# Performance work log

Hardware: AMD Instinct MI355X
Metric: run time of the kernel (lower is better)

Reference implementation:

```python
import jax, jax.numpy as jnp
import numpy as np

B, S, D = 2, 2048, 512
H = 8
G = 4
LAMBDA_INIT = 0.2  # 0.8 - 0.6*exp(-0.3*(layer_idx-1)) with layer_idx=1
EPS = 1e-5


def setup_inputs() -> dict:
    key = jax.random.key(0)
    ks = jax.random.split(key, 16)
    n = jax.random.normal
    return {
        "x": n(ks[0], (B, S, D), jnp.float32),
        "K1_w": n(ks[1], (D, D), jnp.float32) * 0.02,
        "K1_b": n(ks[2], (D,), jnp.float32) * 0.02,
        "Q1_w": n(ks[3], (D, D), jnp.float32) * 0.02,
        "K2_w": n(ks[4], (D, D), jnp.float32) * 0.02,
        "K2_b": n(ks[5], (D,), jnp.float32) * 0.02,
        "Q2_w": n(ks[6], (D, D), jnp.float32) * 0.02,
        "V_w": n(ks[7], (D, D), jnp.float32) * 0.02,
        "lambda_q1": n(ks[8], (H, 1), jnp.float32),
        "lambda_k1": n(ks[9], (H, 1), jnp.float32),
        "lambda_q2": n(ks[10], (H, 1), jnp.float32),
        "lambda_k2": n(ks[11], (H, 1), jnp.float32),
        "gn_w": jnp.ones((D,), jnp.float32),
        "gn_b": jnp.zeros((D,), jnp.float32),
        "out_w": n(ks[12], (D, D), jnp.float32) * 0.02,
        "out_b": n(ks[13], (D,), jnp.float32) * 0.02,
    }


def reference(x, K1_w, K1_b, Q1_w, K2_w, K2_b, Q2_w, V_w,
              lambda_q1, lambda_k1, lambda_q2, lambda_k2,
              gn_w, gn_b, out_w, out_b):
    b, s, d = x.shape
    hd = d // H

    def heads(t):  # (b,s,d) -> (b,H,s,hd)
        return t.reshape(b, s, H, hd).transpose(0, 2, 1, 3)

    q1 = heads(x @ Q1_w.T)
    k1 = heads(x @ K1_w.T + K1_b)
    q2 = heads(x @ Q2_w.T)
    k2 = heads(x @ K2_w.T + K2_b)
    v = heads(x @ V_w.T)

    scale = hd ** 0.5
    a1 = jax.nn.softmax(jnp.einsum('bhqd,bhkd->bhqk', q1, k1) / scale, axis=-1)
    a2 = jax.nn.softmax(jnp.einsum('bhqd,bhkd->bhqk', q2, k2) / scale, axis=-1)

    lam = (jnp.exp(lambda_q1 * lambda_k1)
           - jnp.exp(lambda_q2 * lambda_k2) + LAMBDA_INIT)  # (H,1)
    attn = a1 - lam.reshape(1, H, 1, 1) * a2

    o = jnp.einsum('bhqk,bhkd->bhqd', attn, v)
    o = o.transpose(0, 2, 1, 3).reshape(b, s, d)

    # GroupNorm over channels: input (b, d, s), groups G normalize over (d/G, s)
    xc = o.transpose(0, 2, 1).reshape(b, G, d // G, s)
    mu = xc.mean(axis=(2, 3), keepdims=True)
    var = xc.var(axis=(2, 3), keepdims=True)
    xn = ((xc - mu) * jax.lax.rsqrt(var + EPS)).reshape(b, d, s)
    xn = xn * gn_w[None, :, None] + gn_b[None, :, None]

    y = xn.transpose(0, 2, 1) @ out_w.T + out_b
    return y
```

## Files before the change

kernel.cpp:

```cpp
#include <hip/hip_runtime.h>
#include <hip/hip_bf16.h>

typedef __bf16 bf16;
typedef __attribute__((ext_vector_type(4))) __bf16 bf16x4;
typedef __attribute__((ext_vector_type(8))) __bf16 bf16x8;
typedef __attribute__((ext_vector_type(4))) float f32x4;

#define MFMA16(a, b, c) __builtin_amdgcn_mfma_f32_16x16x32_bf16((a), (b), (c), 0, 0, 0)

static constexpr float EPS = 1e-5f;
static constexpr float LAMBDA_INIT = 0.2f;
static constexpr float LOG2E = 1.44269504088896340736f;

__device__ __forceinline__ bf16x8 cvt8(const float* p) {
    const f32x4 a = *(const f32x4*)p;
    const f32x4 b = *(const f32x4*)(p + 4);
    bf16x8 r;
    r[0] = (bf16)a[0]; r[1] = (bf16)a[1]; r[2] = (bf16)a[2]; r[3] = (bf16)a[3];
    r[4] = (bf16)b[0]; r[5] = (bf16)b[1]; r[6] = (bf16)b[2]; r[7] = (bf16)b[3];
    return r;
}

__device__ __forceinline__ void gload_lds16(const void* g, void* l) {
    __builtin_amdgcn_global_load_lds(
        (const __attribute__((address_space(1))) unsigned int*)g,
        (__attribute__((address_space(3))) unsigned int*)l,
        16, 0, 0);
}

__global__ __launch_bounds__(256) void prep_kernel(
    const float* __restrict__ x,
    const float* __restrict__ q1w, const float* __restrict__ k1w,
    const float* __restrict__ q2w, const float* __restrict__ k2w,
    const float* __restrict__ vw,
    const float* __restrict__ ow, const float* __restrict__ gnw,
    const float* __restrict__ gnb,
    bf16* __restrict__ xb, bf16* __restrict__ wb,
    bf16* __restrict__ owg, float* __restrict__ S0, float* __restrict__ stats)
{
    const int tid = threadIdx.x;
    if (blockIdx.x < 1664) {
        const size_t base = ((size_t)blockIdx.x * 256 + tid) * 8;
        if (base < 2097152) {
            *(bf16x8*)(xb + base) = cvt8(x + base);
        } else {
            const size_t wbase = base - 2097152;
            const int wsel = (int)(wbase >> 18);
            const size_t off = wbase & 262143;
            const float* W = (wsel == 0) ? q1w : (wsel == 1) ? k1w :
                             (wsel == 2) ? q2w : (wsel == 3) ? k2w : vw;
            *(bf16x8*)(wb + wbase) = cvt8(W + off);
        }
        return;
    }

    __shared__ float red[4];
    const int pb = blockIdx.x - 1664;
    if (pb == 0 && tid < 16) stats[tid] = 0.f;

    const int n0 = pb * 16;
    const int c0 = tid, c1 = tid + 256;
    const float gw0 = gnw[c0], gw1 = gnw[c1];
    const float gb0 = gnb[c0], gb1 = gnb[c1];

    for (int n = 0; n < 16; ++n) {
        const size_t rowb = (size_t)(n0 + n) * 512;
        const float w0 = ow[rowb + c0];
        const float w1 = ow[rowb + c1];
        owg[rowb + c0] = (bf16)(w0 * gw0);
        owg[rowb + c1] = (bf16)(w1 * gw1);
        float s = gb0 * w0 + gb1 * w1;
#pragma unroll
        for (int off = 1; off < 64; off <<= 1) s += __shfl_xor(s, off, 64);
        if ((tid & 63) == 0) red[tid >> 6] = s;
        __syncthreads();
        if (tid == 0) S0[n0 + n] = red[0] + red[1] + red[2] + red[3];
        __syncthreads();
    }
}

__global__ __launch_bounds__(256) void proj_kernel(
    const bf16* __restrict__ xb, const bf16* __restrict__ wb,
    const float* __restrict__ k1b, const float* __restrict__ k2b,
    bf16* __restrict__ q1o, bf16* __restrict__ k1o,
    bf16* __restrict__ q2o, bf16* __restrict__ k2o,
    bf16* __restrict__ vto)
{
    __shared__ __align__(16) bf16 sh[32768];
    bf16* const As0 = sh;
    bf16* const As1 = sh + 8192;
    bf16* const Bs0 = sh + 16384;
    bf16* const Bs1 = sh + 24576;

    const int tid = threadIdx.x;
    const int wave = tid >> 6, lane = tid & 63;
    const int l15 = lane & 15, quad = lane >> 4;
    const int wm = wave >> 1, wn = wave & 1;

    const int mb = blockIdx.x / 20;
    const int nb = blockIdx.x % 20;
    const int wsel = nb >> 2;
    const int nrow0 = (nb & 3) * 128;

    const int srow = lane >> 3;
    const int scol = 8 * ((lane & 7) ^ srow);
    const bf16* ag = xb + (size_t)(mb * 128 + srow) * 512 + scol;
    const bf16* bg = wb + (size_t)(wsel * 512 + nrow0 + srow) * 512 + scol;

    f32x4 acc[4][4];
#pragma unroll
    for (int i = 0; i < 4; ++i)
#pragma unroll
        for (int j = 0; j < 4; ++j)
            acc[i][j] = (f32x4){0.f, 0.f, 0.f, 0.f};

#define STAGE_PROJ(abuf, bbuf, s) do {                                         \
    const int k0_ = (s) * 64;                                                  \
    _Pragma("unroll")                                                          \
    for (int c_ = 0; c_ < 4; ++c_) {                                           \
        const int chunk_ = wave * 4 + c_;                                      \
        gload_lds16(ag + (size_t)(chunk_ * 8) * 512 + k0_, (abuf) + chunk_ * 512); \
        gload_lds16(bg + (size_t)(chunk_ * 8) * 512 + k0_, (bbuf) + chunk_ * 512); \
    }                                                                          \
} while (0)

    STAGE_PROJ(As0, Bs0, 0);
    __syncthreads();

    const int ka = 8 * (quad ^ (l15 & 7));

    for (int s = 0; s < 8; ++s) {
        const bf16* Ac = (s & 1) ? As1 : As0;
        const bf16* Bc = (s & 1) ? Bs1 : Bs0;
        if (s < 7) {
            if (s & 1) STAGE_PROJ(As0, Bs0, s + 1);
            else       STAGE_PROJ(As1, Bs1, s + 1);
        }

        bf16x8 al[4], ah[4], bl[4], bh_[4];
#pragma unroll
        for (int i = 0; i < 4; ++i) {
            const bf16* p = Ac + (wm * 64 + i * 16 + l15) * 64;
            al[i] = *(const bf16x8*)(p + ka);
            ah[i] = *(const bf16x8*)(p + (ka ^ 32));
        }
#pragma unroll
        for (int j = 0; j < 4; ++j) {
            const bf16* p = Bc + (wn * 64 + j * 16 + l15) * 64;
            bl[j]  = *(const bf16x8*)(p + ka);
            bh_[j] = *(const bf16x8*)(p + (ka ^ 32));
        }

#pragma unroll
        for (int i = 0; i < 4; ++i)
#pragma unroll
            for (int j = 0; j < 4; ++j) {
                acc[i][j] = MFMA16(al[i], bl[j], acc[i][j]);
                acc[i][j] = MFMA16(ah[i], bh_[j], acc[i][j]);
            }

        __syncthreads();
    }

    const int bidx = mb >> 4;
    const int sbase = (mb & 15) * 128;
    const float scale = (wsel == 0 || wsel == 2) ? 0.125f * LOG2E : 1.0f;

    if (wsel != 4) {
        bf16* const T = sh;
        const int swzq = quad << 4;
#pragma unroll
        for (int j = 0; j < 4; ++j) {
            const int nl = wn * 64 + j * 16 + l15;
            const int ncol = nrow0 + nl;
            float bias = 0.f;
            if (wsel == 1) bias = k1b[ncol];
            if (wsel == 3) bias = k2b[ncol];
            const int nswz = nl ^ swzq;
#pragma unroll
            for (int i = 0; i < 4; ++i) {
                const int mbase = wm * 64 + i * 16 + quad * 4;
#pragma unroll
                for (int r = 0; r < 4; ++r)
                    T[(mbase + r) * 128 + nswz] = (bf16)(acc[i][j][r] * scale + bias);
            }
        }
        __syncthreads();

        bf16* const dst = (wsel == 0) ? q1o : (wsel == 1) ? k1o :
                          (wsel == 2) ? q2o : k2o;
#pragma unroll
        for (int hsel = 0; hsel < 2; ++hsel) {
            const int h = (nrow0 >> 6) + hsel;
            bf16* db = dst + ((size_t)(bidx * 8 + h) * 2048 + sbase) * 64;
#pragma unroll
            for (int ps = 0; ps < 4; ++ps) {
                const int idx = (ps * 256 + tid) * 8;
                const int m = idx >> 6, hd = idx & 63;
                const bf16x8 v = *(const bf16x8*)(
                    T + m * 128 + ((hsel * 64 + hd) ^ (((m >> 2) & 3) << 4)));
                *(bf16x8*)(db + idx) = v;
            }
        }
    } else {
        bf16* const Tt = sh;
#pragma unroll
        for (int j = 0; j < 4; ++j) {
            const int nl = wn * 64 + j * 16 + l15;
            const int hd = (nrow0 + nl) & 63;
            const int xh = (hd >> 1) & 3;
            const int swz = (nl & 7) << 2;
#pragma unroll
            for (int i = 0; i < 4; ++i) {
                const int colb = (wm * 64 + (i >> 1) * 32 + ((quad ^ xh) << 3)
                                  + ((i & 1) << 2)) ^ swz;
                bf16x4 pk;
#pragma unroll
                for (int r = 0; r < 4; ++r) pk[r] = (bf16)acc[i][j][r];
                *(bf16x4*)(Tt + nl * 132 + colb) = pk;
            }
        }
        __syncthreads();

#pragma unroll
        for (int ps = 0; ps < 8; ++ps) {
            const int rown = ps * 16 + (tid >> 4);
            const int seg = tid & 15;
            const int swz = (rown & 7) << 2;
            const bf16x4 lo = *(const bf16x4*)(Tt + rown * 132 + ((seg * 8) ^ swz));
            const bf16x4 hi = *(const bf16x4*)(Tt + rown * 132 + ((seg * 8 + 4) ^ swz));
            const int ncol = nrow0 + rown;
            const int h = ncol >> 6, hd = ncol & 63;
            bf16x8 v;
            v[0] = lo[0]; v[1] = lo[1]; v[2] = lo[2]; v[3] = lo[3];
            v[4] = hi[0]; v[5] = hi[1]; v[6] = hi[2]; v[7] = hi[3];
            *(bf16x8*)(vto + ((size_t)(bidx * 8 + h) * 64 + hd) * 2048
                       + sbase + seg * 8) = v;
        }
    }
#undef STAGE_PROJ
}

__global__ __launch_bounds__(512, 4) void attn_kernel(
    const bf16* __restrict__ q1, const bf16* __restrict__ k1,
    const bf16* __restrict__ q2, const bf16* __restrict__ k2,
    const bf16* __restrict__ vt,
    const float* __restrict__ lq1, const float* __restrict__ lk1,
    const float* __restrict__ lq2, const float* __restrict__ lk2,
    bf16* __restrict__ o, float* __restrict__ stats)
{
    __shared__ __align__(16) bf16 smem[3][12288];
    __shared__ float lbuf[8][2][16];
    __shared__ float sred[8][2];

    const int tid = threadIdx.x;
    const int wave = tid >> 6;
    const int lane = tid & 63;
    const int l15 = lane & 15, quad = lane >> 4;
    const int qtile = wave & 3;
    const int kg = wave >> 2;

    const int rid = (blockIdx.x & 7) * 64 + (blockIdx.x >> 3);
    const int bh = rid >> 5;
    const int qt = rid & 31;
    const int b = bh >> 3, h = bh & 7;

    const bf16* k1t = k1 + (size_t)bh * 2048 * 64;
    const bf16* k2t = k2 + (size_t)bh * 2048 * 64;
    const bf16* vtt = vt + (size_t)bh * 64 * 2048;

    const int qrow = qt * 64 + qtile * 16 + l15;
    const bf16* q1p = q1 + ((size_t)bh * 2048 + qrow) * 64 + quad * 8;
    const bf16* q2p = q2 + ((size_t)bh * 2048 + qrow) * 64 + quad * 8;
    const bf16x8 q1f0 = *(const bf16x8*)(q1p);
    const bf16x8 q1f1 = *(const bf16x8*)(q1p + 32);
    const bf16x8 q2f0 = *(const bf16x8*)(q2p);
    const bf16x8 q2f1 = *(const bf16x8*)(q2p + 32);

    const int sw = wave & 3;
    const int skey0 = (wave < 4) ? 0 : 1024;
    const size_t ksrc0 = (size_t)(skey0 + sw * 8 + (lane >> 3)) * 64
                       + 8 * ((lane & 7) ^ (lane >> 3));
    const size_t vsrc0 = (size_t)(sw * 16 + (lane >> 2)) * 2048 + skey0 + (lane & 3) * 8;

#define STAGE_ATTN(buf, itv) do {                                   \
    const size_t koff_ = ksrc0 + (size_t)(itv) * 32 * 64;           \
    gload_lds16(k1t + koff_, (buf) + wave * 512);                   \
    gload_lds16(k2t + koff_, (buf) + 4096 + wave * 512);            \
    gload_lds16(vtt + vsrc0 + (itv) * 32, (buf) + 8192 + wave * 512); \
} while (0)

    const int koffa = 8 * (quad ^ (l15 & 7));
    const int koffb = 8 * ((quad + 4) ^ (l15 & 7));
    const int vsw = 8 * (quad ^ ((l15 >> 1) & 3));

    f32x4 O1[4], O2[4];
    float l1 = 0.f, l2 = 0.f;
#pragma unroll
    for (int t = 0; t < 4; ++t) {
        O1[t] = (f32x4){0.f, 0.f, 0.f, 0.f};
        O2[t] = (f32x4){0.f, 0.f, 0.f, 0.f};
    }

    STAGE_ATTN(smem[0], 0);
    STAGE_ATTN(smem[1], 1);

    int cur = 0;
    for (int it = 0; it < 32; ++it) {
        if (it < 31) {
            asm volatile("s_waitcnt vmcnt(3)\ns_barrier" ::: "memory");
        } else {
            asm volatile("s_waitcnt vmcnt(0)\ns_barrier" ::: "memory");
        }
        __builtin_amdgcn_sched_barrier(0);

        const bf16* sb = smem[cur];
        const int n2 = (cur == 0) ? 2 : cur - 1;
        if (it < 30) STAGE_ATTN(smem[n2], it + 2);

        const bf16* k1r = sb + kg * 2048;
        const bf16* k2r = sb + 4096 + kg * 2048;
        const bf16* vr  = sb + 8192 + kg * 2048;

        const bf16x8 k1t0a = *(const bf16x8*)(k1r + l15 * 64 + koffa);
        const bf16x8 k1t0b = *(const bf16x8*)(k1r + l15 * 64 + koffb);
        const bf16x8 k1t1a = *(const bf16x8*)(k1r + (16 + l15) * 64 + koffa);
        const bf16x8 k1t1b = *(const bf16x8*)(k1r + (16 + l15) * 64 + koffb);
        const bf16x8 k2t0a = *(const bf16x8*)(k2r + l15 * 64 + koffa);
        const bf16x8 k2t0b = *(const bf16x8*)(k2r + l15 * 64 + koffb);
        const bf16x8 k2t1a = *(const bf16x8*)(k2r + (16 + l15) * 64 + koffa);
        const bf16x8 k2t1b = *(const bf16x8*)(k2r + (16 + l15) * 64 + koffb);
        const bf16x8 v0 = *(const bf16x8*)(vr + l15 * 32 + vsw);
        const bf16x8 v1 = *(const bf16x8*)(vr + (16 + l15) * 32 + vsw);
        const bf16x8 v2 = *(const bf16x8*)(vr + (32 + l15) * 32 + vsw);
        const bf16x8 v3 = *(const bf16x8*)(vr + (48 + l15) * 32 + vsw);

        const f32x4 z = (f32x4){0.f, 0.f, 0.f, 0.f};
        __builtin_amdgcn_s_setprio(1);
        f32x4 s1t0 = MFMA16(k1t0a, q1f0, z);  s1t0 = MFMA16(k1t0b, q1f1, s1t0);
        f32x4 s1t1 = MFMA16(k1t1a, q1f0, z);  s1t1 = MFMA16(k1t1b, q1f1, s1t1);
        f32x4 s2t0 = MFMA16(k2t0a, q2f0, z);  s2t0 = MFMA16(k2t0b, q2f1, s2t0);
        f32x4 s2t1 = MFMA16(k2t1a, q2f0, z);  s2t1 = MFMA16(k2t1b, q2f1, s2t1);
        __builtin_amdgcn_s_setprio(0);

        bf16x8 b1, b2;
#pragma unroll
        for (int r = 0; r < 4; ++r) {
            float e;
            e = __builtin_amdgcn_exp2f(s1t0[r]); l1 += e; b1[r]     = (bf16)e;
            e = __builtin_amdgcn_exp2f(s1t1[r]); l1 += e; b1[4 + r] = (bf16)e;
            e = __builtin_amdgcn_exp2f(s2t0[r]); l2 += e; b2[r]     = (bf16)e;
            e = __builtin_amdgcn_exp2f(s2t1[r]); l2 += e; b2[4 + r] = (bf16)e;
        }

        __builtin_amdgcn_s_setprio(1);
        O1[0] = MFMA16(v0, b1, O1[0]);
        O1[1] = MFMA16(v1, b1, O1[1]);
        O1[2] = MFMA16(v2, b1, O1[2]);
        O1[3] = MFMA16(v3, b1, O1[3]);
        O2[0] = MFMA16(v0, b2, O2[0]);
        O2[1] = MFMA16(v1, b2, O2[1]);
        O2[2] = MFMA16(v2, b2, O2[2]);
        O2[3] = MFMA16(v3, b2, O2[3]);
        __builtin_amdgcn_s_setprio(0);

        cur = (cur == 2) ? 0 : cur + 1;
    }

    l1 += __shfl_xor(l1, 16, 64);  l1 += __shfl_xor(l1, 32, 64);
    l2 += __shfl_xor(l2, 16, 64);  l2 += __shfl_xor(l2, 32, 64);
    if (lane < 16) {
        lbuf[wave][0][lane] = l1;
        lbuf[wave][1][lane] = l2;
    }
    __syncthreads();

    f32x4* rb = (f32x4*)smem;
    if (wave == 4 || wave == 5) {
        f32x4* dst = rb + (wave - 4) * 512;
#pragma unroll
        for (int t = 0; t < 4; ++t) {
            dst[t * 64 + lane]       = O1[t];
            dst[(4 + t) * 64 + lane] = O2[t];
        }
    }
    __syncthreads();
    if (wave == 0 || wave == 1) {
        const f32x4* src = rb + wave * 512;
#pragma unroll
        for (int t = 0; t < 4; ++t) {
            O1[t] += src[t * 64 + lane];
            O2[t] += src[(4 + t) * 64 + lane];
        }
    }
    __syncthreads();
    if (wave == 6 || wave == 7) {
        f32x4* dst = rb + (wave - 6) * 512;
#pragma unroll
        for (int t = 0; t < 4; ++t) {
            dst[t * 64 + lane]       = O1[t];
            dst[(4 + t) * 64 + lane] = O2[t];
        }
    }
    __syncthreads();
    if (wave == 2 || wave == 3) {
        const f32x4* src = rb + (wave - 2) * 512;
#pragma unroll
        for (int t = 0; t < 4; ++t) {
            O1[t] += src[t * 64 + lane];
            O2[t] += src[(4 + t) * 64 + lane];
        }
    }

    float ssum = 0.f, ssq = 0.f;
    if (wave < 4) {
        const float L1 = l1 + lbuf[wave + 4][0][l15];
        const float L2 = l2 + lbuf[wave + 4][1][l15];
        const float lam = __expf(lq1[h] * lk1[h]) - __expf(lq2[h] * lk2[h]) + LAMBDA_INIT;
        const float inv1 = 1.f / L1;
        const float inv2 = lam / L2;
        const size_t row = (size_t)(b * 2048 + qt * 64 + wave * 16 + l15) * 512 + h * 64;
#pragma unroll
        for (int t = 0; t < 4; ++t) {
#pragma unroll
            for (int r = 0; r < 4; ++r) {
                const float val = O1[t][r] * inv1 - O2[t][r] * inv2;
                ssum += val;
                ssq += val * val;
                o[row + t * 16 + quad * 4 + r] = (bf16)val;
            }
        }
    }
#pragma unroll
    for (int off = 1; off < 64; off <<= 1) {
        ssum += __shfl_xor(ssum, off, 64);
        ssq += __shfl_xor(ssq, off, 64);
    }
    if (lane == 0) { sred[wave][0] = ssum; sred[wave][1] = ssq; }
    __syncthreads();
    if (tid == 0) {
        float s0 = 0.f, s1 = 0.f;
        for (int w = 0; w < 8; ++w) { s0 += sred[w][0]; s1 += sred[w][1]; }
        const int bg = b * 4 + (h >> 1);
        atomicAdd(&stats[bg * 2], s0);
        atomicAdd(&stats[bg * 2 + 1], s1);
    }
#undef STAGE_ATTN
}

__global__ __launch_bounds__(256) void out_gemm_kernel(
    const bf16* __restrict__ o, const bf16* __restrict__ owg,
    const float* __restrict__ S0, const float* __restrict__ stats,
    const float* __restrict__ ob, float* __restrict__ y)
{
    __shared__ __align__(16) bf16 sh[24576];

    const int tid = threadIdx.x;
    const int wave = tid >> 6, lane = tid & 63;
    const int l15 = lane & 15, quad = lane >> 4;

    const int mb = blockIdx.x >> 3;
    const int nb = blockIdx.x & 7;
    const int b = mb >> 5;

    const float N = 128.f * 2048.f;
    float mu[4], rs[4];
#pragma unroll
    for (int g = 0; g < 4; ++g) {
        const float m = stats[(b * 4 + g) * 2] / N;
        const float var = stats[(b * 4 + g) * 2 + 1] / N - m * m;
        mu[g] = m;
        rs[g] = rsqrtf(var + EPS);
    }

    const int srow = lane >> 3;
    const int scol = 8 * ((lane & 7) ^ srow);
    const bf16* ag = o + (size_t)(mb * 64 + srow) * 512 + scol;
    const bf16* bg = owg + (size_t)(nb * 64 + srow) * 512 + scol;

#define STAGE_OUT(abuf, bbuf, s) do {                                          \
    const int k0_ = (s) * 64;                                                  \
    _Pragma("unroll")                                                          \
    for (int c_ = 0; c_ < 2; ++c_) {                                           \
        const int chunk_ = wave * 2 + c_;                                      \
        gload_lds16(ag + (size_t)(chunk_ * 8) * 512 + k0_, (abuf) + chunk_ * 512); \
        gload_lds16(bg + (size_t)(chunk_ * 8) * 512 + k0_, (bbuf) + chunk_ * 512); \
    }                                                                          \
} while (0)

    f32x4 acc[4], tot[4];
#pragma unroll
    for (int i = 0; i < 4; ++i) {
        acc[i] = (f32x4){0.f, 0.f, 0.f, 0.f};
        tot[i] = (f32x4){0.f, 0.f, 0.f, 0.f};
    }
    float s1g[4];
    float s1p = 0.f;
#pragma unroll
    for (int g = 0; g < 4; ++g) s1g[g] = 0.f;

    STAGE_OUT(sh, sh + 12288, 0);
    STAGE_OUT(sh + 4096, sh + 12288 + 4096, 1);

    const int ka = 8 * (quad ^ (l15 & 7));

    int cur = 0;
    for (int kk = 0; kk < 8; ++kk) {
        if (kk < 7) {
            asm volatile("s_waitcnt vmcnt(4)\ns_barrier" ::: "memory");
        } else {
            asm volatile("s_waitcnt vmcnt(0)\ns_barrier" ::: "memory");
        }
        __builtin_amdgcn_sched_barrier(0);

        const bf16* Ac = sh + cur * 4096;
        const bf16* Bc = sh + 12288 + cur * 4096;
        const int n2 = (cur == 0) ? 2 : cur - 1;
        if (kk < 6) STAGE_OUT(sh + n2 * 4096, sh + 12288 + n2 * 4096, kk + 2);

        bf16x8 al[4], ah[4];
#pragma unroll
        for (int i = 0; i < 4; ++i) {
            const bf16* p = Ac + (i * 16 + l15) * 64;
            al[i] = *(const bf16x8*)(p + ka);
            ah[i] = *(const bf16x8*)(p + (ka ^ 32));
        }
        const bf16* pb = Bc + (wave * 16 + l15) * 64;
        const bf16x8 bl = *(const bf16x8*)(pb + ka);
        const bf16x8 bh = *(const bf16x8*)(pb + (ka ^ 32));

#pragma unroll
        for (int i = 0; i < 4; ++i) {
            acc[i] = MFMA16(al[i], bl, acc[i]);
            acc[i] = MFMA16(ah[i], bh, acc[i]);
        }

#pragma unroll
        for (int j = 0; j < 8; ++j) s1p += (float)bl[j] + (float)bh[j];

        if (kk & 1) {
            const int g = kk >> 1;
#pragma unroll
            for (int i = 0; i < 4; ++i) {
#pragma unroll
                for (int r = 0; r < 4; ++r) tot[i][r] += rs[g] * acc[i][r];
                acc[i] = (f32x4){0.f, 0.f, 0.f, 0.f};
            }
            float sg = s1p + __shfl_xor(s1p, 16, 64);
            sg += __shfl_xor(sg, 32, 64);
            s1g[g] = sg;
            s1p = 0.f;
        }

        cur = (cur == 2) ? 0 : cur + 1;
    }
    __syncthreads();

    const int ncol = nb * 64 + wave * 16 + l15;
    float bias = S0[ncol] + ob[ncol];
#pragma unroll
    for (int g = 0; g < 4; ++g) bias -= mu[g] * rs[g] * s1g[g];

    float* const Tf = (float*)sh;
    const int nl = wave * 16 + l15;
#pragma unroll
    for (int i = 0; i < 4; ++i) {
        const int mbase = i * 16 + quad * 4;
#pragma unroll
        for (int r = 0; r < 4; ++r)
            Tf[(mbase + r) * 64 + (nl ^ (quad << 4))] = tot[i][r] + bias;
    }
    __syncthreads();

#pragma unroll
    for (int ps = 0; ps < 4; ++ps) {
        const int idx = (ps * 256 + tid) * 4;
        const int m = idx >> 6, n4 = idx & 63;
        const f32x4 v = *(const f32x4*)(Tf + m * 64 + (n4 ^ (((m >> 2) & 3) << 4)));
        *(f32x4*)(y + (size_t)(mb * 64 + m) * 512 + nb * 64 + n4) = v;
    }
#undef STAGE_OUT
}

extern "C" void kernel_launch(void* const* d_in, const int* in_sizes, int n_in,
                              void* d_out, int out_size, void* d_ws, size_t ws_size,
                              hipStream_t stream)
{
    const float* x   = (const float*)d_in[0];
    const float* K1w = (const float*)d_in[1];
    const float* K1b = (const float*)d_in[2];
    const float* Q1w = (const float*)d_in[3];
    const float* K2w = (const float*)d_in[4];
    const float* K2b = (const float*)d_in[5];
    const float* Q2w = (const float*)d_in[6];
    const float* Vw  = (const float*)d_in[7];
    const float* lq1 = (const float*)d_in[8];
    const float* lk1 = (const float*)d_in[9];
    const float* lq2 = (const float*)d_in[10];
    const float* lk2 = (const float*)d_in[11];
    const float* gnw = (const float*)d_in[12];
    const float* gnb = (const float*)d_in[13];
    const float* Ow  = (const float*)d_in[14];
    const float* Ob  = (const float*)d_in[15];

    const size_t SZ = (size_t)2 * 8 * 2048 * 64;
    bf16* q1 = (bf16*)d_ws;
    bf16* k1 = q1 + SZ;
    bf16* q2 = k1 + SZ;
    bf16* k2 = q2 + SZ;
    bf16* vt = k2 + SZ;
    bf16* o  = vt + SZ;
    bf16* xb = o;
    bf16* wb = o + SZ;
    bf16* owg = wb + (size_t)2560 * 512;
    float* S0 = (float*)(owg + 512 * 512);
    float* stats = S0 + 512;

    prep_kernel<<<1696, 256, 0, stream>>>(x, Q1w, K1w, Q2w, K2w, Vw,
                                          Ow, gnw, gnb, xb, wb, owg, S0, stats);
    proj_kernel<<<640, 256, 0, stream>>>(xb, wb, K1b, K2b,
                                         q1, k1, q2, k2, vt);
    attn_kernel<<<512, 512, 0, stream>>>(q1, k1, q2, k2, vt,
                                         lq1, lk1, lq2, lk2, o, stats);
    out_gemm_kernel<<<512, 256, 0, stream>>>(o, owg, S0, stats, Ob,
                                             (float*)d_out);
}
```

Baseline: 174.6 us.

## Split attention waves by stream and query pair, switch to double-buffered K/V staging

```diff
diff --git a/kernel.cpp b/kernel.cpp
--- a/kernel.cpp
+++ b/kernel.cpp
@@ -249,16 +249,18 @@
     const float* __restrict__ lq2, const float* __restrict__ lk2,
     bf16* __restrict__ o, float* __restrict__ stats)
 {
-    __shared__ __align__(16) bf16 smem[3][12288];
+    __shared__ __align__(16) bf16 smem[2][12288];
     __shared__ float lbuf[8][2][16];
-    __shared__ float sred[8][2];
+    __shared__ float sred[2][2];
 
     const int tid = threadIdx.x;
     const int wave = tid >> 6;
     const int lane = tid & 63;
     const int l15 = lane & 15, quad = lane >> 4;
-    const int qtile = wave & 3;
     const int kg = wave >> 2;
+    const int w4 = wave & 3;
+    const int qp = w4 & 1;
+    const int st = w4 >> 1;
 
     const int rid = (blockIdx.x & 7) * 64 + (blockIdx.x >> 3);
     const int bh = rid >> 5;
@@ -269,13 +271,13 @@
     const bf16* k2t = k2 + (size_t)bh * 2048 * 64;
     const bf16* vtt = vt + (size_t)bh * 64 * 2048;
 
-    const int qrow = qt * 64 + qtile * 16 + l15;
-    const bf16* q1p = q1 + ((size_t)bh * 2048 + qrow) * 64 + quad * 8;
-    const bf16* q2p = q2 + ((size_t)bh * 2048 + qrow) * 64 + quad * 8;
-    const bf16x8 q1f0 = *(const bf16x8*)(q1p);
-    const bf16x8 q1f1 = *(const bf16x8*)(q1p + 32);
-    const bf16x8 q2f0 = *(const bf16x8*)(q2p);
-    const bf16x8 q2f1 = *(const bf16x8*)(q2p + 32);
+    const bf16* qs = st ? q2 : q1;
+    const int qrowA = qt * 64 + qp * 32 + l15;
+    const bf16* qpA = qs + ((size_t)bh * 2048 + qrowA) * 64 + quad * 8;
+    const bf16x8 qA0 = *(const bf16x8*)(qpA);
+    const bf16x8 qA1 = *(const bf16x8*)(qpA + 32);
+    const bf16x8 qB0 = *(const bf16x8*)(qpA + 16 * 64);
+    const bf16x8 qB1 = *(const bf16x8*)(qpA + 16 * 64 + 32);
 
     const int sw = wave & 3;
     const int skey0 = (wave < 4) ? 0 : 1024;
@@ -294,42 +296,28 @@
     const int koffb = 8 * ((quad + 4) ^ (l15 & 7));
     const int vsw = 8 * (quad ^ ((l15 >> 1) & 3));
 
-    f32x4 O1[4], O2[4];
-    float l1 = 0.f, l2 = 0.f;
+    f32x4 OA[4], OB[4];
+    float lA = 0.f, lB = 0.f;
 #pragma unroll
     for (int t = 0; t < 4; ++t) {
-        O1[t] = (f32x4){0.f, 0.f, 0.f, 0.f};
-        O2[t] = (f32x4){0.f, 0.f, 0.f, 0.f};
+        OA[t] = (f32x4){0.f, 0.f, 0.f, 0.f};
+        OB[t] = (f32x4){0.f, 0.f, 0.f, 0.f};
     }
 
     STAGE_ATTN(smem[0], 0);
-    STAGE_ATTN(smem[1], 1);
-
-    int cur = 0;
+    __syncthreads();
+
     for (int it = 0; it < 32; ++it) {
-        if (it < 31) {
-            asm volatile("s_waitcnt vmcnt(3)\ns_barrier" ::: "memory");
-        } else {
-            asm volatile("s_waitcnt vmcnt(0)\ns_barrier" ::: "memory");
-        }
-        __builtin_amdgcn_sched_barrier(0);
-
-        const bf16* sb = smem[cur];
-        const int n2 = (cur == 0) ? 2 : cur - 1;
-        if (it < 30) STAGE_ATTN(smem[n2], it + 2);
-
-        const bf16* k1r = sb + kg * 2048;
-        const bf16* k2r = sb + 4096 + kg * 2048;
-        const bf16* vr  = sb + 8192 + kg * 2048;
-
-        const bf16x8 k1t0a = *(const bf16x8*)(k1r + l15 * 64 + koffa);
-        const bf16x8 k1t0b = *(const bf16x8*)(k1r + l15 * 64 + koffb);
-        const bf16x8 k1t1a = *(const bf16x8*)(k1r + (16 + l15) * 64 + koffa);
-        const bf16x8 k1t1b = *(const bf16x8*)(k1r + (16 + l15) * 64 + koffb);
-        const bf16x8 k2t0a = *(const bf16x8*)(k2r + l15 * 64 + koffa);
-        const bf16x8 k2t0b = *(const bf16x8*)(k2r + l15 * 64 + koffb);
-        const bf16x8 k2t1a = *(const bf16x8*)(k2r + (16 + l15) * 64 + koffa);
-        const bf16x8 k2t1b = *(const bf16x8*)(k2r + (16 + l15) * 64 + koffb);
+        const bf16* sb = smem[it & 1];
+        if (it < 31) STAGE_ATTN(smem[(it & 1) ^ 1], it + 1);
+
+        const bf16* kr = sb + st * 4096 + kg * 2048;
+        const bf16* vr = sb + 8192 + kg * 2048;
+
+        const bf16x8 kt0a = *(const bf16x8*)(kr + l15 * 64 + koffa);
+        const bf16x8 kt0b = *(const bf16x8*)(kr + l15 * 64 + koffb);
+        const bf16x8 kt1a = *(const bf16x8*)(kr + (16 + l15) * 64 + koffa);
+        const bf16x8 kt1b = *(const bf16x8*)(kr + (16 + l15) * 64 + koffb);
         const bf16x8 v0 = *(const bf16x8*)(vr + l15 * 32 + vsw);
         const bf16x8 v1 = *(const bf16x8*)(vr + (16 + l15) * 32 + vsw);
         const bf16x8 v2 = *(const bf16x8*)(vr + (32 + l15) * 32 + vsw);
@@ -337,97 +325,98 @@
 
         const f32x4 z = (f32x4){0.f, 0.f, 0.f, 0.f};
         __builtin_amdgcn_s_setprio(1);
-        f32x4 s1t0 = MFMA16(k1t0a, q1f0, z);  s1t0 = MFMA16(k1t0b, q1f1, s1t0);
-        f32x4 s1t1 = MFMA16(k1t1a, q1f0, z);  s1t1 = MFMA16(k1t1b, q1f1, s1t1);
-        f32x4 s2t0 = MFMA16(k2t0a, q2f0, z);  s2t0 = MFMA16(k2t0b, q2f1, s2t0);
-        f32x4 s2t1 = MFMA16(k2t1a, q2f0, z);  s2t1 = MFMA16(k2t1b, q2f1, s2t1);
+        f32x4 sA0 = MFMA16(kt0a, qA0, z);  sA0 = MFMA16(kt0b, qA1, sA0);
+        f32x4 sA1 = MFMA16(kt1a, qA0, z);  sA1 = MFMA16(kt1b, qA1, sA1);
+        f32x4 sB0 = MFMA16(kt0a, qB0, z);  sB0 = MFMA16(kt0b, qB1, sB0);
+        f32x4 sB1 = MFMA16(kt1a, qB0, z);  sB1 = MFMA16(kt1b, qB1, sB1);
         __builtin_amdgcn_s_setprio(0);
 
-        bf16x8 b1, b2;
+        bf16x8 bA, bB;
 #pragma unroll
         for (int r = 0; r < 4; ++r) {
             float e;
-            e = __builtin_amdgcn_exp2f(s1t0[r]); l1 += e; b1[r]     = (bf16)e;
-            e = __builtin_amdgcn_exp2f(s1t1[r]); l1 += e; b1[4 + r] = (bf16)e;
-            e = __builtin_amdgcn_exp2f(s2t0[r]); l2 += e; b2[r]     = (bf16)e;
-            e = __builtin_amdgcn_exp2f(s2t1[r]); l2 += e; b2[4 + r] = (bf16)e;
+            e = __builtin_amdgcn_exp2f(sA0[r]); lA += e; bA[r]     = (bf16)e;
+            e = __builtin_amdgcn_exp2f(sA1[r]); lA += e; bA[4 + r] = (bf16)e;
+            e = __builtin_amdgcn_exp2f(sB0[r]); lB += e; bB[r]     = (bf16)e;
+            e = __builtin_amdgcn_exp2f(sB1[r]); lB += e; bB[4 + r] = (bf16)e;
         }
 
         __builtin_amdgcn_s_setprio(1);
-        O1[0] = MFMA16(v0, b1, O1[0]);
-        O1[1] = MFMA16(v1, b1, O1[1]);
-        O1[2] = MFMA16(v2, b1, O1[2]);
-        O1[3] = MFMA16(v3, b1, O1[3]);
-        O2[0] = MFMA16(v0, b2, O2[0]);
-        O2[1] = MFMA16(v1, b2, O2[1]);
-        O2[2] = MFMA16(v2, b2, O2[2]);
-        O2[3] = MFMA16(v3, b2, O2[3]);
+        OA[0] = MFMA16(v0, bA, OA[0]);
+        OA[1] = MFMA16(v1, bA, OA[1]);
+        OA[2] = MFMA16(v2, bA, OA[2]);
+        OA[3] = MFMA16(v3, bA, OA[3]);
+        OB[0] = MFMA16(v0, bB, OB[0]);
+        OB[1] = MFMA16(v1, bB, OB[1]);
+        OB[2] = MFMA16(v2, bB, OB[2]);
+        OB[3] = MFMA16(v3, bB, OB[3]);
         __builtin_amdgcn_s_setprio(0);
 
-        cur = (cur == 2) ? 0 : cur + 1;
-    }
-
-    l1 += __shfl_xor(l1, 16, 64);  l1 += __shfl_xor(l1, 32, 64);
-    l2 += __shfl_xor(l2, 16, 64);  l2 += __shfl_xor(l2, 32, 64);
+        __syncthreads();
+    }
+
+    lA += __shfl_xor(lA, 16, 64);  lA += __shfl_xor(lA, 32, 64);
+    lB += __shfl_xor(lB, 16, 64);  lB += __shfl_xor(lB, 32, 64);
     if (lane < 16) {
-        lbuf[wave][0][lane] = l1;
-        lbuf[wave][1][lane] = l2;
+        lbuf[wave][0][lane] = lA;
+        lbuf[wave][1][lane] = lB;
     }
     __syncthreads();
 
     f32x4* rb = (f32x4*)smem;
-    if (wave == 4 || wave == 5) {
-        f32x4* dst = rb + (wave - 4) * 512;
+    if (kg == 1) {
+        f32x4* dst = rb + w4 * 512;
 #pragma unroll
         for (int t = 0; t < 4; ++t) {
-            dst[t * 64 + lane]       = O1[t];
-            dst[(4 + t) * 64 + lane] = O2[t];
-        }
-    }
-    __syncthreads();
-    if (wave == 0 || wave == 1) {
-        const f32x4* src = rb + wave * 512;
+            dst[t * 64 + lane]       = OA[t];
+            dst[(4 + t) * 64 + lane] = OB[t];
+        }
+    }
+    __syncthreads();
+    if (kg == 0) {
+        const f32x4* src = rb + w4 * 512;
 #pragma unroll
         for (int t = 0; t < 4; ++t) {
-            O1[t] += src[t * 64 + lane];
-            O2[t] += src[(4 + t) * 64 + lane];
-        }
-    }
-    __syncthreads();
-    if (wave == 6 || wave == 7) {
-        f32x4* dst = rb + (wave - 6) * 512;
+            OA[t] += src[t * 64 + lane];
+            OB[t] += src[(4 + t) * 64 + lane];
+        }
+    }
+    __syncthreads();
+
+    if (kg == 0 && st == 1) {
+        f32x4* dst = rb + qp * 512;
 #pragma unroll
         for (int t = 0; t < 4; ++t) {
-            dst[t * 64 + lane]       = O1[t];
-            dst[(4 + t) * 64 + lane] = O2[t];
-        }
-    }
-    __syncthreads();
-    if (wave == 2 || wave == 3) {
-        const f32x4* src = rb + (wave - 2) * 512;
+            dst[t * 64 + lane]       = OA[t];
+            dst[(4 + t) * 64 + lane] = OB[t];
+        }
+    }
+    __syncthreads();
+
+    float ssum = 0.f, ssq = 0.f;
+    if (kg == 0 && st == 0) {
+        const f32x4* src = rb + qp * 512;
+        const float L1A = lA + lbuf[4 + qp][0][l15];
+        const float L1B = lB + lbuf[4 + qp][1][l15];
+        const float L2A = lbuf[2 + qp][0][l15] + lbuf[6 + qp][0][l15];
+        const float L2B = lbuf[2 + qp][1][l15] + lbuf[6 + qp][1][l15];
+        const float lam = __expf(lq1[h] * lk1[h]) - __expf(lq2[h] * lk2[h]) + LAMBDA_INIT;
+        const float i1A = 1.f / L1A, i2A = lam / L2A;
+        const float i1B = 1.f / L1B, i2B = lam / L2B;
+        const size_t rowA = (size_t)(b * 2048 + qt * 64 + qp * 32 + l15) * 512 + h * 64;
+        const size_t rowB = rowA + 16 * 512;
 #pragma unroll
         for (int t = 0; t < 4; ++t) {
-            O1[t] += src[t * 64 + lane];
-            O2[t] += src[(4 + t) * 64 + lane];
-        }
-    }
-
-    float ssum = 0.f, ssq = 0.f;
-    if (wave < 4) {
-        const float L1 = l1 + lbuf[wave + 4][0][l15];
-        const float L2 = l2 + lbuf[wave + 4][1][l15];
-        const float lam = __expf(lq1[h] * lk1[h]) - __expf(lq2[h] * lk2[h]) + LAMBDA_INIT;
-        const float inv1 = 1.f / L1;
-        const float inv2 = lam / L2;
-        const size_t row = (size_t)(b * 2048 + qt * 64 + wave * 16 + l15) * 512 + h * 64;
-#pragma unroll
-        for (int t = 0; t < 4; ++t) {
+            const f32x4 o2A = src[t * 64 + lane];
+            const f32x4 o2B = src[(4 + t) * 64 + lane];
 #pragma unroll
             for (int r = 0; r < 4; ++r) {
-                const float val = O1[t][r] * inv1 - O2[t][r] * inv2;
-                ssum += val;
-                ssq += val * val;
-                o[row + t * 16 + quad * 4 + r] = (bf16)val;
+                const float vA = OA[t][r] * i1A - o2A[r] * i2A;
+                const float vB = OB[t][r] * i1B - o2B[r] * i2B;
+                ssum += vA + vB;
+                ssq += vA * vA + vB * vB;
+                o[rowA + t * 16 + quad * 4 + r] = (bf16)vA;
+                o[rowB + t * 16 + quad * 4 + r] = (bf16)vB;
             }
         }
     }
@@ -436,11 +425,11 @@
         ssum += __shfl_xor(ssum, off, 64);
         ssq += __shfl_xor(ssq, off, 64);
     }
-    if (lane == 0) { sred[wave][0] = ssum; sred[wave][1] = ssq; }
+    if (kg == 0 && st == 0 && lane == 0) { sred[qp][0] = ssum; sred[qp][1] = ssq; }
     __syncthreads();
     if (tid == 0) {
-        float s0 = 0.f, s1 = 0.f;
-        for (int w = 0; w < 8; ++w) { s0 += sred[w][0]; s1 += sred[w][1]; }
+        const float s0 = sred[0][0] + sred[1][0];
+        const float s1 = sred[0][1] + sred[1][1];
         const int bg = b * 4 + (h >> 1);
         atomicAdd(&stats[bg * 2], s0);
         atomicAdd(&stats[bg * 2 + 1], s1);
@@ -507,9 +496,9 @@
     int cur = 0;
     for (int kk = 0; kk < 8; ++kk) {
         if (kk < 7) {
-            asm volatile("s_waitcnt vmcnt(4)\ns_barrier" ::: "memory");
+            asm volatile("s_waitcnt vmcnt(4) lgkmcnt(0)\ns_barrier" ::: "memory");
         } else {
-            asm volatile("s_waitcnt vmcnt(0)\ns_barrier" ::: "memory");
+            asm volatile("s_waitcnt vmcnt(0) lgkmcnt(0)\ns_barrier" ::: "memory");
         }
         __builtin_amdgcn_sched_barrier(0);
 
```

New measurement: 171.5 us. No clear change (-1.8%).
